# Kernel optimization log

Hardware: AMD Instinct MI355X
Metric: run time of the kernel (lower is better)

Reference implementation:

```python
import jax, jax.numpy as jnp
import numpy as np

B, T, D = 8, 4096, 256
K = 8192  # codebook_size


def setup_inputs() -> dict:
    key = jax.random.key(0)
    k1, k2 = jax.random.split(key)
    h = jax.random.normal(k1, (B, T, D), dtype=jnp.float32)
    # nn.init.uniform_(codebook.weight, -1.0, 1.0)
    codebook = jax.random.uniform(k2, (K, D), dtype=jnp.float32, minval=-1.0, maxval=1.0)
    return {"h": h, "codebook": codebook}


def reference(h, codebook):
    b, t, d = h.shape
    flat = h.reshape(-1, d)                              # [N, D]
    x2 = jnp.sum(flat * flat, axis=1, keepdims=True)     # [N, 1]
    c2 = jnp.sum(codebook * codebook, axis=1)[None, :]   # [1, K]
    xc = flat @ codebook.T                               # [N, K]
    dist = x2 + c2 - 2.0 * xc                            # [N, K]
    idx_flat = jnp.argmin(dist, axis=1)                  # [N] int
    q_flat = codebook[idx_flat]                          # gather [N, D]
    q = q_flat.reshape(b, t, d)
    idx = idx_flat.reshape(b, t)
    # straight-through estimator
    q_ste = h + jax.lax.stop_gradient(q - h)
    return q_ste, idx
```

## Files before the change

### kernel.cpp

```cpp
#include <hip/hip_runtime.h>

typedef short short8 __attribute__((ext_vector_type(8)));
typedef float f32x4 __attribute__((ext_vector_type(4)));

#define DIMS   256
#define KCODES 8192
#define NTOK   32768
#define BM     64
#define BN     64
#define NTILES 128
#define MARGIN 0.75f
#define CAP    6144

__device__ __forceinline__ unsigned short f2bf(float f) {
    unsigned u = __builtin_bit_cast(unsigned, f);
    unsigned r = (u + 0x7FFFu + ((u >> 16) & 1u)) >> 16;
    return (unsigned short)r;
}
__device__ __forceinline__ unsigned fenc(float f) {
    unsigned u = __builtin_bit_cast(unsigned, f);
    return ((int)u >= 0) ? (u | 0x80000000u) : ~u;
}

__global__ __launch_bounds__(256) void prep_kernel(const float* __restrict__ cb,
                                                   float* __restrict__ c2,
                                                   unsigned short* __restrict__ cbbf,
                                                   int do_conv) {
    const int g    = blockIdx.x * 4 + (threadIdx.x >> 6);
    const int lane = threadIdx.x & 63;
    const int l15  = lane & 15;
    const int quad = lane >> 4;
    const float* rp = cb + (size_t)(g * 16 + l15) * DIMS + quad * 8;
    float ss = 0.f;
#pragma unroll
    for (int kk = 0; kk < 8; kk++) {
        float4 v0 = *(const float4*)(rp + kk * 32);
        float4 v1 = *(const float4*)(rp + kk * 32 + 4);
        ss += v0.x * v0.x + v0.y * v0.y + v0.z * v0.z + v0.w * v0.w
            + v1.x * v1.x + v1.y * v1.y + v1.z * v1.z + v1.w * v1.w;
        if (do_conv) {
            short8 s;
            s[0] = f2bf(v0.x); s[1] = f2bf(v0.y); s[2] = f2bf(v0.z); s[3] = f2bf(v0.w);
            s[4] = f2bf(v1.x); s[5] = f2bf(v1.y); s[6] = f2bf(v1.z); s[7] = f2bf(v1.w);
            *(short8*)(cbbf + (size_t)g * 4096 + kk * 512 + lane * 8) = s;
        }
    }
    ss += __shfl_xor(ss, 16);
    ss += __shfl_xor(ss, 32);
    if (quad == 0) c2[g * 16 + l15] = ss;
}

template <bool WSBF>
__global__ __launch_bounds__(512, 4) void vq_main(const float* __restrict__ h,
                                                  const float* __restrict__ cb,
                                                  const unsigned short* __restrict__ cbbf,
                                                  const float* __restrict__ c2g,
                                                  float* __restrict__ out_q,
                                                  float* __restrict__ out_idx) {
    __shared__ unsigned mrun[BM];
    __shared__ unsigned list[CAP];
    __shared__ unsigned long long best64[BM];
    __shared__ int cnt;

    const int tid  = threadIdx.x;
    const int lane = tid & 63;
    const int wave = tid >> 6;
    const int l15  = lane & 15;
    const int quad = lane >> 4;
    const int wm   = wave >> 2;
    const int wn   = wave & 3;
    const int tokBase = blockIdx.x * BM;

    if (tid < BM) mrun[tid] = 0x7F7FFFFFu;
    if (tid == 0) cnt = 0;

    short8 afr[2][8];
#pragma unroll
    for (int i = 0; i < 2; i++) {
        const float* base = h + (size_t)(tokBase + wm * 32 + i * 16 + l15) * DIMS + quad * 8;
#pragma unroll
        for (int kk = 0; kk < 8; kk++) {
            float4 v0 = *(const float4*)(base + kk * 32);
            float4 v1 = *(const float4*)(base + kk * 32 + 4);
            short8 s;
            s[0] = f2bf(v0.x); s[1] = f2bf(v0.y); s[2] = f2bf(v0.z); s[3] = f2bf(v0.w);
            s[4] = f2bf(v1.x); s[5] = f2bf(v1.y); s[6] = f2bf(v1.z); s[7] = f2bf(v1.w);
            afr[i][kk] = s;
        }
    }

    __syncthreads();

    short8 bfr[8];
    const char* fb = (const char*)cbbf + (size_t)wn * 8192 + (size_t)lane * 16;
    auto loadB = [&](int t) {
        if constexpr (WSBF) {
            const char* p = fb + (size_t)t * 32768;
#pragma unroll
            for (int n = 0; n < 8; n++)
                bfr[n] = *(const short8*)(p + n * 1024);
        } else {
            const float* rp = cb + (size_t)(t * BN + wn * 16 + l15) * DIMS + quad * 8;
#pragma unroll
            for (int kk = 0; kk < 8; kk++) {
                float4 v0 = *(const float4*)(rp + kk * 32);
                float4 v1 = *(const float4*)(rp + kk * 32 + 4);
                short8 s;
                s[0] = f2bf(v0.x); s[1] = f2bf(v0.y); s[2] = f2bf(v0.z); s[3] = f2bf(v0.w);
                s[4] = f2bf(v1.x); s[5] = f2bf(v1.y); s[6] = f2bf(v1.z); s[7] = f2bf(v1.w);
                bfr[kk] = s;
            }
        }
    };
    loadB(0);

#pragma unroll 1
    for (int it = 0; it <= NTILES; ++it) {
        const int t = (it == NTILES) ? 0 : it;
        const bool haveThr = (it > 0);
        float thr0 = 0.f, thr1 = 0.f;
        if (haveThr) {
            thr0 = __builtin_bit_cast(float, mrun[wm * 32 + l15]) + MARGIN;
            thr1 = __builtin_bit_cast(float, mrun[wm * 32 + 16 + l15]) + MARGIN;
        }
        const int cbase = t * BN + wn * 16;
        const float4 cc = *(const float4*)(c2g + cbase + quad * 4);

        f32x4 acc[2][2];
        acc[0][0] = (f32x4){0,0,0,0}; acc[0][1] = (f32x4){0,0,0,0};
        acc[1][0] = (f32x4){0,0,0,0}; acc[1][1] = (f32x4){0,0,0,0};

        __builtin_amdgcn_s_setprio(1);
#pragma unroll
        for (int kk = 0; kk < 4; kk++) {
            short8 b0 = bfr[kk];
            short8 b1 = bfr[kk + 4];
            acc[0][0] = __builtin_amdgcn_mfma_f32_16x16x32_bf16(b0, afr[0][kk],     acc[0][0], 0, 0, 0);
            acc[1][0] = __builtin_amdgcn_mfma_f32_16x16x32_bf16(b0, afr[1][kk],     acc[1][0], 0, 0, 0);
            acc[0][1] = __builtin_amdgcn_mfma_f32_16x16x32_bf16(b1, afr[0][kk + 4], acc[0][1], 0, 0, 0);
            acc[1][1] = __builtin_amdgcn_mfma_f32_16x16x32_bf16(b1, afr[1][kk + 4], acc[1][1], 0, 0, 0);
        }
        __builtin_amdgcn_s_setprio(0);

        if (it < NTILES) loadB((it + 1 == NTILES) ? 0 : it + 1);

        const int code00 = cbase + quad * 4;
#pragma unroll
        for (int i = 0; i < 2; i++) {
            const int tok = wm * 32 + i * 16 + l15;
            const float th = i ? thr1 : thr0;
            float s0 = fmaf(-2.f, acc[i][0][0], fmaf(-2.f, acc[i][1][0], cc.x));
            float s1 = fmaf(-2.f, acc[i][0][1], fmaf(-2.f, acc[i][1][1], cc.y));
            float s2 = fmaf(-2.f, acc[i][0][2], fmaf(-2.f, acc[i][1][2], cc.z));
            float s3 = fmaf(-2.f, acc[i][0][3], fmaf(-2.f, acc[i][1][3], cc.w));
            float vm = fminf(fminf(s0, s1), fminf(s2, s3));
            if (haveThr) {
                const unsigned tk = (unsigned)(tok << 13);
                if (s0 <= th) { int p = atomicAdd(&cnt, 1); if (p < CAP) list[p] = tk | (unsigned)(code00 + 0); }
                if (s1 <= th) { int p = atomicAdd(&cnt, 1); if (p < CAP) list[p] = tk | (unsigned)(code00 + 1); }
                if (s2 <= th) { int p = atomicAdd(&cnt, 1); if (p < CAP) list[p] = tk | (unsigned)(code00 + 2); }
                if (s3 <= th) { int p = atomicAdd(&cnt, 1); if (p < CAP) list[p] = tk | (unsigned)(code00 + 3); }
            }
            if (it < NTILES) {
                vm = fminf(vm, __shfl_xor(vm, 16));
                vm = fminf(vm, __shfl_xor(vm, 32));
                if (quad == 0) atomicMin(&mrun[tok], __builtin_bit_cast(unsigned, vm));
            }
        }
    }
    __syncthreads();

    if (tid < BM) best64[tid] = ~0ULL;
    __syncthreads();

    int n = cnt; if (n > CAP) n = CAP;
    for (int p = wave; p < n; p += 8) {
        unsigned e = list[p];
        int tok = (int)(e >> 13), code = (int)(e & 8191);
        float4 hv = *(const float4*)(h + (size_t)(tokBase + tok) * DIMS + lane * 4);
        float4 cv = *(const float4*)(cb + (size_t)code * DIMS + lane * 4);
        float d = hv.x * cv.x + hv.y * cv.y + hv.z * cv.z + hv.w * cv.w;
#pragma unroll
        for (int m = 1; m < 64; m <<= 1) d += __shfl_xor(d, m);
        float s = c2g[code] - 2.f * d;
        if (lane == 0)
            atomicMin(&best64[tok], ((unsigned long long)fenc(s) << 32) | (unsigned)code);
    }
    __syncthreads();

    if (tid < BM)
        out_idx[tokBase + tid] = (float)(unsigned)(best64[tid] & 0xFFFFFFFFULL);
#pragma unroll
    for (int e = tid; e < BM * (DIMS / 4); e += 512) {
        int r = e >> 6, c4 = e & 63;
        int idx = (int)(unsigned)(best64[r] & 0xFFFFFFFFULL);
        float4 v = *(const float4*)(cb + (size_t)idx * DIMS + c4 * 4);
        *(float4*)(out_q + (size_t)(tokBase + r) * DIMS + c4 * 4) = v;
    }
}

extern "C" void kernel_launch(void* const* d_in, const int* in_sizes, int n_in,
                              void* d_out, int out_size, void* d_ws, size_t ws_size,
                              hipStream_t stream) {
    const float* h  = (const float*)d_in[0];
    const float* cb = (const float*)d_in[1];
    float* out_q   = (float*)d_out;
    float* out_idx = (float*)d_out + (size_t)NTOK * DIMS;

    float* c2 = (float*)d_ws;
    unsigned short* cbbf = (unsigned short*)((char*)d_ws + 32768);
    const size_t needed = 32768 + (size_t)KCODES * DIMS * 2;
    const int wsbf = (ws_size >= needed) ? 1 : 0;

    prep_kernel<<<KCODES / 16 / 4, 256, 0, stream>>>(cb, c2, cbbf, wsbf);
    if (wsbf)
        vq_main<true><<<NTOK / BM, 512, 0, stream>>>(h, cb, cbbf, c2, out_q, out_idx);
    else
        vq_main<false><<<NTOK / BM, 512, 0, stream>>>(h, cb, (const unsigned short*)nullptr, c2, out_q, out_idx);
}
```

Measured before the change: 409.3 us.

## Halve token tile per block and double-buffer codebook fragments across tiles

Shrinks the per-block token tile from 64 to 32, so each wave handles 16 tokens with one A fragment instead of two, and the grid doubles in size. Codebook B fragments now alternate between two register buffers in a manually unrolled two-tile loop, so the next tile's load is issued further ahead of its MFMA use. This aims to raise occupancy and hide global-load latency. The cost is half the reuse of each codebook fragment across tokens, which doubles total codebook traffic, plus more blocks doing the rescoring epilogue.

After: 488.0 us. 1.19x slower.

```diff
diff --git a/kernel.cpp b/kernel.cpp
--- a/kernel.cpp
+++ b/kernel.cpp
@@ -6,11 +6,11 @@
 #define DIMS   256
 #define KCODES 8192
 #define NTOK   32768
-#define BM     64
+#define BM     32
 #define BN     64
 #define NTILES 128
 #define MARGIN 0.75f
-#define CAP    6144
+#define CAP    3072
 
 __device__ __forceinline__ unsigned short f2bf(float f) {
     unsigned u = __builtin_bit_cast(unsigned, f);
@@ -67,107 +67,101 @@
     const int wave = tid >> 6;
     const int l15  = lane & 15;
     const int quad = lane >> 4;
-    const int wm   = wave >> 2;
+    const int wTok = wave >> 2;
     const int wn   = wave & 3;
+    const int tok  = wTok * 16 + l15;
     const int tokBase = blockIdx.x * BM;
 
     if (tid < BM) mrun[tid] = 0x7F7FFFFFu;
     if (tid == 0) cnt = 0;
 
-    short8 afr[2][8];
-#pragma unroll
-    for (int i = 0; i < 2; i++) {
-        const float* base = h + (size_t)(tokBase + wm * 32 + i * 16 + l15) * DIMS + quad * 8;
+    short8 bfA[8], bfB[8];
+    const char* fb = (const char*)cbbf + (size_t)wn * 8192 + (size_t)lane * 16;
+
+#define LOADB(BF, T) do {                                                          \
+        if constexpr (WSBF) {                                                      \
+            const char* p_ = fb + (size_t)(T) * 32768;                             \
+            _Pragma("unroll")                                                      \
+            for (int n_ = 0; n_ < 8; n_++)                                         \
+                BF[n_] = *(const short8*)(p_ + n_ * 1024);                         \
+        } else {                                                                   \
+            const float* rp_ = cb + (size_t)((T) * BN + wn * 16 + l15) * DIMS + quad * 8; \
+            _Pragma("unroll")                                                      \
+            for (int kk_ = 0; kk_ < 8; kk_++) {                                    \
+                float4 v0_ = *(const float4*)(rp_ + kk_ * 32);                     \
+                float4 v1_ = *(const float4*)(rp_ + kk_ * 32 + 4);                 \
+                short8 s_;                                                         \
+                s_[0] = f2bf(v0_.x); s_[1] = f2bf(v0_.y); s_[2] = f2bf(v0_.z); s_[3] = f2bf(v0_.w); \
+                s_[4] = f2bf(v1_.x); s_[5] = f2bf(v1_.y); s_[6] = f2bf(v1_.z); s_[7] = f2bf(v1_.w); \
+                BF[kk_] = s_;                                                      \
+            }                                                                      \
+        }                                                                          \
+    } while (0)
+
+    LOADB(bfA, 0);
+
+    short8 afr[8];
+    {
+        const float* abase = h + (size_t)(tokBase + tok) * DIMS + quad * 8;
 #pragma unroll
         for (int kk = 0; kk < 8; kk++) {
-            float4 v0 = *(const float4*)(base + kk * 32);
-            float4 v1 = *(const float4*)(base + kk * 32 + 4);
+            float4 v0 = *(const float4*)(abase + kk * 32);
+            float4 v1 = *(const float4*)(abase + kk * 32 + 4);
             short8 s;
             s[0] = f2bf(v0.x); s[1] = f2bf(v0.y); s[2] = f2bf(v0.z); s[3] = f2bf(v0.w);
             s[4] = f2bf(v1.x); s[5] = f2bf(v1.y); s[6] = f2bf(v1.z); s[7] = f2bf(v1.w);
-            afr[i][kk] = s;
+            afr[kk] = s;
         }
     }
 
-    __syncthreads();
-
-    short8 bfr[8];
-    const char* fb = (const char*)cbbf + (size_t)wn * 8192 + (size_t)lane * 16;
-    auto loadB = [&](int t) {
-        if constexpr (WSBF) {
-            const char* p = fb + (size_t)t * 32768;
-#pragma unroll
-            for (int n = 0; n < 8; n++)
-                bfr[n] = *(const short8*)(p + n * 1024);
-        } else {
-            const float* rp = cb + (size_t)(t * BN + wn * 16 + l15) * DIMS + quad * 8;
-#pragma unroll
-            for (int kk = 0; kk < 8; kk++) {
-                float4 v0 = *(const float4*)(rp + kk * 32);
-                float4 v1 = *(const float4*)(rp + kk * 32 + 4);
-                short8 s;
-                s[0] = f2bf(v0.x); s[1] = f2bf(v0.y); s[2] = f2bf(v0.z); s[3] = f2bf(v0.w);
-                s[4] = f2bf(v1.x); s[5] = f2bf(v1.y); s[6] = f2bf(v1.z); s[7] = f2bf(v1.w);
-                bfr[kk] = s;
-            }
-        }
-    };
-    loadB(0);
-
+    LOADB(bfB, 1);
+    __syncthreads();
+
+#define TILE(BF, T, TN, PF, USETHR, UPD) do {                                      \
+        const int t_ = (T);                                                        \
+        const int cbase_ = t_ * BN + wn * 16;                                      \
+        float thr_ = 0.f;                                                          \
+        if (USETHR) thr_ = __builtin_bit_cast(float, mrun[tok]) + MARGIN;          \
+        const float4 cc_ = *(const float4*)(c2g + cbase_ + quad * 4);              \
+        f32x4 a0_ = (f32x4){0, 0, 0, 0}, a1_ = (f32x4){0, 0, 0, 0};                \
+        __builtin_amdgcn_s_setprio(1);                                             \
+        _Pragma("unroll")                                                          \
+        for (int kk_ = 0; kk_ < 4; kk_++) {   \
+            a0_ = __builtin_amdgcn_mfma_f32_16x16x32_bf16(BF[kk_],     afr[kk_],     a0_, 0, 0, 0); \
+            a1_ = __builtin_amdgcn_mfma_f32_16x16x32_bf16(BF[kk_ + 4], afr[kk_ + 4], a1_, 0, 0, 0); \
+        }                                                                          \
+        __builtin_amdgcn_s_setprio(0);                                             \
+        if (PF) LOADB(BF, TN);          \
+        const int code00_ = cbase_ + quad * 4;                                     \
+        float s0_ = fmaf(-2.f, a0_[0], fmaf(-2.f, a1_[0], cc_.x));                 \
+        float s1_ = fmaf(-2.f, a0_[1], fmaf(-2.f, a1_[1], cc_.y));                 \
+        float s2_ = fmaf(-2.f, a0_[2], fmaf(-2.f, a1_[2], cc_.z));                 \
+        float s3_ = fmaf(-2.f, a0_[3], fmaf(-2.f, a1_[3], cc_.w));                 \
+        if (USETHR) {                                                              \
+            const unsigned tk_ = (unsigned)(tok << 13);                            \
+            if (s0_ <= thr_) { int p_ = atomicAdd(&cnt, 1); if (p_ < CAP) list[p_] = tk_ | (unsigned)(code00_ + 0); } \
+            if (s1_ <= thr_) { int p_ = atomicAdd(&cnt, 1); if (p_ < CAP) list[p_] = tk_ | (unsigned)(code00_ + 1); } \
+            if (s2_ <= thr_) { int p_ = atomicAdd(&cnt, 1); if (p_ < CAP) list[p_] = tk_ | (unsigned)(code00_ + 2); } \
+            if (s3_ <= thr_) { int p_ = atomicAdd(&cnt, 1); if (p_ < CAP) list[p_] = tk_ | (unsigned)(code00_ + 3); } \
+        }                                                                          \
+        if (UPD) {                                                                 \
+            float vm_ = fminf(fminf(s0_, s1_), fminf(s2_, s3_));                   \
+            vm_ = fminf(vm_, __shfl_xor(vm_, 16));                                 \
+            vm_ = fminf(vm_, __shfl_xor(vm_, 32));                                 \
+                     \
+            if (quad == 0) atomicMin(&mrun[tok], __builtin_bit_cast(unsigned, vm_)); \
+        }                                                                          \
+    } while (0)
+
+    TILE(bfA, 0, 2, true, false, true);
+    TILE(bfB, 1, 3, true, true,  true);
 #pragma unroll 1
-    for (int it = 0; it <= NTILES; ++it) {
-        const int t = (it == NTILES) ? 0 : it;
-        const bool haveThr = (it > 0);
-        float thr0 = 0.f, thr1 = 0.f;
-        if (haveThr) {
-            thr0 = __builtin_bit_cast(float, mrun[wm * 32 + l15]) + MARGIN;
-            thr1 = __builtin_bit_cast(float, mrun[wm * 32 + 16 + l15]) + MARGIN;
-        }
-        const int cbase = t * BN + wn * 16;
-        const float4 cc = *(const float4*)(c2g + cbase + quad * 4);
-
-        f32x4 acc[2][2];
-        acc[0][0] = (f32x4){0,0,0,0}; acc[0][1] = (f32x4){0,0,0,0};
-        acc[1][0] = (f32x4){0,0,0,0}; acc[1][1] = (f32x4){0,0,0,0};
-
-        __builtin_amdgcn_s_setprio(1);
-#pragma unroll
-        for (int kk = 0; kk < 4; kk++) {
-            short8 b0 = bfr[kk];
-            short8 b1 = bfr[kk + 4];
-            acc[0][0] = __builtin_amdgcn_mfma_f32_16x16x32_bf16(b0, afr[0][kk],     acc[0][0], 0, 0, 0);
-            acc[1][0] = __builtin_amdgcn_mfma_f32_16x16x32_bf16(b0, afr[1][kk],     acc[1][0], 0, 0, 0);
-            acc[0][1] = __builtin_amdgcn_mfma_f32_16x16x32_bf16(b1, afr[0][kk + 4], acc[0][1], 0, 0, 0);
-            acc[1][1] = __builtin_amdgcn_mfma_f32_16x16x32_bf16(b1, afr[1][kk + 4], acc[1][1], 0, 0, 0);
-        }
-        __builtin_amdgcn_s_setprio(0);
-
-        if (it < NTILES) loadB((it + 1 == NTILES) ? 0 : it + 1);
-
-        const int code00 = cbase + quad * 4;
-#pragma unroll
-        for (int i = 0; i < 2; i++) {
-            const int tok = wm * 32 + i * 16 + l15;
-            const float th = i ? thr1 : thr0;
-            float s0 = fmaf(-2.f, acc[i][0][0], fmaf(-2.f, acc[i][1][0], cc.x));
-            float s1 = fmaf(-2.f, acc[i][0][1], fmaf(-2.f, acc[i][1][1], cc.y));
-            float s2 = fmaf(-2.f, acc[i][0][2], fmaf(-2.f, acc[i][1][2], cc.z));
-            float s3 = fmaf(-2.f, acc[i][0][3], fmaf(-2.f, acc[i][1][3], cc.w));
-            float vm = fminf(fminf(s0, s1), fminf(s2, s3));
-            if (haveThr) {
-                const unsigned tk = (unsigned)(tok << 13);
-                if (s0 <= th) { int p = atomicAdd(&cnt, 1); if (p < CAP) list[p] = tk | (unsigned)(code00 + 0); }
-                if (s1 <= th) { int p = atomicAdd(&cnt, 1); if (p < CAP) list[p] = tk | (unsigned)(code00 + 1); }
-                if (s2 <= th) { int p = atomicAdd(&cnt, 1); if (p < CAP) list[p] = tk | (unsigned)(code00 + 2); }
-                if (s3 <= th) { int p = atomicAdd(&cnt, 1); if (p < CAP) list[p] = tk | (unsigned)(code00 + 3); }
-            }
-            if (it < NTILES) {
-                vm = fminf(vm, __shfl_xor(vm, 16));
-                vm = fminf(vm, __shfl_xor(vm, 32));
-                if (quad == 0) atomicMin(&mrun[tok], __builtin_bit_cast(unsigned, vm));
-            }
-        }
-    }
+    for (int t2 = 1; t2 < 64; ++t2) {
+        TILE(bfA, 2 * t2,     (2 * t2 + 2) & 127, true,       true, true);
+        TILE(bfB, 2 * t2 + 1, 2 * t2 + 3,         (t2 < 63),  true, true);
+    }
+    TILE(bfA, 0, 0, false, true, false);
+
     __syncthreads();
 
     if (tid < BM) best64[tid] = ~0ULL;
@@ -176,15 +170,15 @@
     int n = cnt; if (n > CAP) n = CAP;
     for (int p = wave; p < n; p += 8) {
         unsigned e = list[p];
-        int tok = (int)(e >> 13), code = (int)(e & 8191);
-        float4 hv = *(const float4*)(h + (size_t)(tokBase + tok) * DIMS + lane * 4);
+        int tk = (int)(e >> 13), code = (int)(e & 8191);
+        float4 hv = *(const float4*)(h + (size_t)(tokBase + tk) * DIMS + lane * 4);
         float4 cv = *(const float4*)(cb + (size_t)code * DIMS + lane * 4);
         float d = hv.x * cv.x + hv.y * cv.y + hv.z * cv.z + hv.w * cv.w;
 #pragma unroll
         for (int m = 1; m < 64; m <<= 1) d += __shfl_xor(d, m);
         float s = c2g[code] - 2.f * d;
         if (lane == 0)
-            atomicMin(&best64[tok], ((unsigned long long)fenc(s) << 32) | (unsigned)code);
+            atomicMin(&best64[tk], ((unsigned long long)fenc(s) << 32) | (unsigned)code);
     }
     __syncthreads();
 
@@ -197,6 +191,8 @@
         float4 v = *(const float4*)(cb + (size_t)idx * DIMS + c4 * 4);
         *(float4*)(out_q + (size_t)(tokBase + r) * DIMS + c4 * 4) = v;
     }
+#undef TILE
+#undef LOADB
 }
 
 extern "C" void kernel_launch(void* const* d_in, const int* in_sizes, int n_in,
```
